# Kernel tuning notes

Measured on AMD Instinct MI355X. Metric: run time of the kernel, lower is better.

Reference implementation:

```python
import jax, jax.numpy as jnp
import numpy as np

B, H, W, D, SD, K, CD, ITERS = 16, 64, 64, 64, 64, 5, 8, 4
N = H * W
EPS = 1e-8
SCALE = SD ** -0.5

def _ln(x, g, b, eps=1e-5):
    m = jnp.mean(x, -1, keepdims=True)
    v = jnp.mean(jnp.square(x - m), -1, keepdims=True)
    return (x - m) * jax.lax.rsqrt(v + eps) * g + b

def _grid():
    xs = jnp.linspace(-1.0, 1.0, W)
    ys = jnp.linspace(-1.0, 1.0, H)
    yy, xx = jnp.meshgrid(ys, xs, indexing='ij')
    return jnp.stack([xx, yy], -1).reshape(N, 2)  # (N,2)

def _gru(x, h, wih, whh, bih, bhh):
    # PyTorch GRUCell: gates in (r, z, n) order
    gi = x @ wih.T + bih
    gh = h @ whh.T + bhh
    ir, iz, i_n = jnp.split(gi, 3, -1)
    hr, hz, h_n = jnp.split(gh, 3, -1)
    r = jax.nn.sigmoid(ir + hr)
    z = jax.nn.sigmoid(iz + hz)
    n = jnp.tanh(i_n + r * h_n)
    return (1.0 - z) * n + z * h

def _forward(p):
    grid = _grid()
    feat = _ln(p['feat'].reshape(B, N, D), p['ln_feat_g'], p['ln_feat_b'])
    fc = _ln(p['feat_color'], p['ln_fc_g'], p['ln_fc_b'])
    # background k/v: position-independent, computed once outside the loop
    ge_bg = jnp.concatenate([grid, -grid], -1) @ p['w_grid'].T + p['b_grid']  # (N,D)
    k_bg = _ln(feat @ p['w_kbg'].T + ge_bg, p['ln_bg_g'], p['ln_bg_b']) @ p['w_mlp_bg'].T + p['b_mlp_bg']
    v_bg = _ln(feat @ p['w_vbg'].T + ge_bg, p['ln_bg_g'], p['ln_bg_b']) @ p['w_mlp_bg'].T + p['b_mlp_bg']
    slot_fg = jnp.broadcast_to(p['slots_init_fg'], (B, K - 1, SD))
    slot_bg = jnp.broadcast_to(p['slots_init_bg'], (B, 1, SD))
    pos = jnp.broadcast_to(p['fg_position'], (B, K - 1, 2))
    kf = feat @ p['w_kfg'].T  # position-independent fg parts
    vf = feat @ p['w_vfg'].T
    for it in range(ITERS):
        q_fg = _ln(slot_fg, p['ln_q_g'], p['ln_q_b']) @ p['w_q'].T          # (B,K-1,SD)
        q_bg = _ln(slot_bg, p['ln_qbg_g'], p['ln_qbg_b']) @ p['w_qbg'].T    # (B,1,SD)
        rel = grid[None, None] - pos[:, :, None]                            # (B,K-1,N,2)
        ge = jnp.concatenate([rel, -rel], -1) @ p['w_grid'].T + p['b_grid'] # (B,K-1,N,D)
        k = _ln(kf[:, None] + ge, p['ln_fg_g'], p['ln_fg_b']) @ p['w_mlp_fg'].T + p['b_mlp_fg']
        v = _ln(vf[:, None] + ge, p['ln_fg_g'], p['ln_fg_b']) @ p['w_mlp_fg'].T + p['b_mlp_fg']
        a_fg = jnp.einsum('bkd,bknd->bkn', q_fg, k) * SCALE
        a_bg = jnp.einsum('bd,bnd->bn', q_bg[:, 0], k_bg) * SCALE
        # non-standard softmax: normalize across slot axis (K), not tokens
        attn = jax.nn.softmax(jnp.concatenate([a_bg[:, None], a_fg], 1), axis=1) + EPS
        w_fg = attn[:, 1:] / jnp.sum(attn[:, 1:], -1, keepdims=True)        # (B,K-1,N)
        w_bg = attn[:, :1] / jnp.sum(attn[:, :1], -1, keepdims=True)        # (B,1,N)
        pos = jnp.einsum('bkn,nd->bkd', w_fg, grid)
        pos = jnp.clip(pos + jnp.tanh(w_fg @ p['w_pos'].T + p['b_pos']) / 5.0, -1.0, 1.0)
        if it != ITERS - 1:
            upd_fg = jnp.einsum('bkn,bknd->bkd', w_fg, v)
            upd_bg = jnp.einsum('bkn,bnd->bkd', w_bg, v_bg)
            slot_fg = _gru(upd_fg.reshape(-1, SD), slot_fg.reshape(-1, SD),
                           p['gfg_wih'], p['gfg_whh'], p['gfg_bih'], p['gfg_bhh']).reshape(B, K - 1, SD)
            slot_fg = slot_fg + _ln(slot_fg, p['ln_rfg_g'], p['ln_rfg_b']) @ p['w_rfg'].T + p['b_rfg']
            slot_bg = _gru(upd_bg.reshape(-1, SD), slot_bg.reshape(-1, SD),
                           p['gbg_wih'], p['gbg_whh'], p['gbg_bih'], p['gbg_bhh']).reshape(B, 1, SD)
            slot_bg = slot_bg + _ln(slot_bg, p['ln_rbg_g'], p['ln_rbg_b']) @ p['w_rbg'].T + p['b_rbg']
        else:
            # last iteration: slots = [visual update, color update]
            slot_fg = jnp.concatenate([jnp.einsum('bkn,bknd->bkd', w_fg, v),
                                       jnp.einsum('bkn,bnd->bkd', w_fg, fc)], -1)
            slot_bg = jnp.concatenate([jnp.einsum('bkn,bnd->bkd', w_bg, v_bg),
                                       jnp.einsum('bkn,bnd->bkd', w_bg, fc)], -1)
    return jnp.concatenate([slot_bg, slot_fg], 1)  # (B,K,SD+CD)

def setup_inputs():
    key = jax.random.key(0)
    ks = iter(jax.random.split(key, 64))
    def rn(shape, s=0.02):
        return jax.random.normal(next(ks), shape, dtype=jnp.float32) * s
    inp = {
        'feat': jax.random.normal(next(ks), (B, H, W, D), dtype=jnp.float32),
        'feat_color': jax.random.normal(next(ks), (B, N, CD), dtype=jnp.float32),
        'w_grid': rn((D, 4)), 'b_grid': rn((D,)),
        'w_kfg': rn((D, D)), 'w_vfg': rn((D, D)),
        'w_kbg': rn((D, D)), 'w_vbg': rn((D, D)),
        'ln_fg_g': jnp.ones((D,)), 'ln_fg_b': jnp.zeros((D,)),
        'w_mlp_fg': rn((SD, D)), 'b_mlp_fg': rn((SD,)),
        'ln_bg_g': jnp.ones((D,)), 'ln_bg_b': jnp.zeros((D,)),
        'w_mlp_bg': rn((SD, D)), 'b_mlp_bg': rn((SD,)),
        'slots_init_fg': rn((1, K - 1, SD), 0.5),
        'slots_init_bg': rn((1, 1, SD), 0.5),
        'fg_position': jax.random.uniform(next(ks), (1, K - 1, 2), dtype=jnp.float32, minval=-0.75, maxval=0.75),
        'w_pos': rn((2, N), 0.001), 'b_pos': jnp.zeros((2,)),
        'ln_q_g': jnp.ones((SD,)), 'ln_q_b': jnp.zeros((SD,)), 'w_q': rn((SD, SD)),
        'ln_qbg_g': jnp.ones((SD,)), 'ln_qbg_b': jnp.zeros((SD,)), 'w_qbg': rn((SD, SD)),
        'gfg_wih': rn((3 * SD, SD)), 'gfg_whh': rn((3 * SD, SD)),
        'gfg_bih': rn((3 * SD,)), 'gfg_bhh': rn((3 * SD,)),
        'gbg_wih': rn((3 * SD, SD)), 'gbg_whh': rn((3 * SD, SD)),
        'gbg_bih': rn((3 * SD,)), 'gbg_bhh': rn((3 * SD,)),
        'ln_rfg_g': jnp.ones((SD,)), 'ln_rfg_b': jnp.zeros((SD,)),
        'w_rfg': rn((SD, SD)), 'b_rfg': rn((SD,)),
        'ln_rbg_g': jnp.ones((SD,)), 'ln_rbg_b': jnp.zeros((SD,)),
        'w_rbg': rn((SD, SD)), 'b_rbg': rn((SD,)),
        'ln_feat_g': jnp.ones((D,)), 'ln_feat_b': jnp.zeros((D,)),
        'ln_fc_g': jnp.ones((CD,)), 'ln_fc_b': jnp.zeros((CD,)),
    }
    return inp

def reference(feat, feat_color, w_grid, b_grid, w_kfg, w_vfg, w_kbg, w_vbg,
              ln_fg_g, ln_fg_b, w_mlp_fg, b_mlp_fg, ln_bg_g, ln_bg_b, w_mlp_bg, b_mlp_bg,
              slots_init_fg, slots_init_bg, fg_position, w_pos, b_pos,
              ln_q_g, ln_q_b, w_q, ln_qbg_g, ln_qbg_b, w_qbg,
              gfg_wih, gfg_whh, gfg_bih, gfg_bhh, gbg_wih, gbg_whh, gbg_bih, gbg_bhh,
              ln_rfg_g, ln_rfg_b, w_rfg, b_rfg, ln_rbg_g, ln_rbg_b, w_rbg, b_rbg,
              ln_feat_g, ln_feat_b, ln_fc_g, ln_fc_b):
    p = dict(locals())
    return _forward(p)
```

## Files before the change

kernel.cpp:

```cpp
#include <hip/hip_runtime.h>
#include <math.h>
#include <stddef.h>

#define NB 16
#define ND 64
#define NN 4096
#define NCD 8
#define NITER 4
#define ATT_EPS 1e-8f
#define LNEPS 1e-5f
#define QSCALE 0.125f

static constexpr size_t SZ_MAT   = (size_t)NB*NN*ND;
static constexpr size_t OFF_UK   = 0;
static constexpr size_t OFF_CV0  = OFF_UK   + SZ_MAT;
static constexpr size_t OFF_XKBG = OFF_CV0  + SZ_MAT;
static constexpr size_t OFF_XVBG = OFF_XKBG + SZ_MAT;
static constexpr size_t OFF_SCAL = OFF_XVBG + SZ_MAT;
static constexpr size_t OFF_ACC  = OFF_SCAL + (size_t)NB*NN*8;
static constexpr size_t OFF_SFG  = OFF_ACC  + (size_t)NB*448;
static constexpr size_t OFF_SBG  = OFF_SFG  + (size_t)NB*256;
static constexpr size_t OFF_POS  = OFF_SBG  + (size_t)NB*64;
static constexpr size_t OFF_QW   = OFF_POS  + (size_t)NB*8;
static constexpr size_t OFF_QWBG = OFF_QW   + (size_t)NB*256;
static constexpr size_t OFF_QBBG = OFF_QWBG + (size_t)NB*64;
static constexpr size_t OFF_ABC  = OFF_QBBG + (size_t)NB;
static constexpr size_t OFF_CXG  = OFF_ABC  + (size_t)NB*16;
static constexpr size_t OFF_CYG  = OFF_CXG  + 64;
static constexpr size_t OFF_GS   = OFF_CYG  + 64;

#define A_S 0
#define A_W0 8
#define A_WX 12
#define A_WY 16
#define A_P 24
#define A_T 32
#define A_C 40
#define A_Y 80
#define A_YBG 336
#define ACC_STRIDE 448

__device__ __forceinline__ float g16sum(float x){
  x += __shfl_xor(x, 1);
  x += __shfl_xor(x, 2);
  x += __shfl_xor(x, 4);
  x += __shfl_xor(x, 8);
  return x;
}
__device__ __forceinline__ float wavesum(float x){
  x += __shfl_xor(x, 1);  x += __shfl_xor(x, 2);
  x += __shfl_xor(x, 4);  x += __shfl_xor(x, 8);
  x += __shfl_xor(x, 16); x += __shfl_xor(x, 32);
  return x;
}
__device__ __forceinline__ float4 f4fma(float a, float4 w, float4 c){
  c.x = fmaf(a, w.x, c.x); c.y = fmaf(a, w.y, c.y);
  c.z = fmaf(a, w.z, c.z); c.w = fmaf(a, w.w, c.w);
  return c;
}
__device__ __forceinline__ float dot4(float4 a, float4 b){
  return fmaf(a.x,b.x, fmaf(a.y,b.y, fmaf(a.z,b.z, a.w*b.w)));
}
__device__ __forceinline__ float4 ln16v(float4 x, float4 g, float4 bb){
  float m = g16sum(x.x + x.y + x.z + x.w) * (1.0f/64.0f);
  float4 c = make_float4(x.x - m, x.y - m, x.z - m, x.w - m);
  float var = g16sum(c.x*c.x + c.y*c.y + c.z*c.z + c.w*c.w) * (1.0f/64.0f);
  float rs = rsqrtf(var + LNEPS);
  return make_float4(c.x*rs*g.x + bb.x, c.y*rs*g.y + bb.y,
                     c.z*rs*g.z + bb.z, c.w*rs*g.w + bb.w);
}
__device__ __forceinline__ float rowdot64(const float* __restrict__ W, const float* x){
  const float4* w4 = (const float4*)W;
  const float4* x4 = (const float4*)x;
  float s = 0.0f;
  #pragma unroll
  for (int t = 0; t < 16; ++t){
    float4 w = w4[t], xx = x4[t];
    s = fmaf(w.x,xx.x, fmaf(w.y,xx.y, fmaf(w.z,xx.z, fmaf(w.w,xx.w, s))));
  }
  return s;
}
#define XRED(x) do { x += __shfl_xor(x, 16); x += __shfl_xor(x, 32); } while (0)

__global__ __launch_bounds__(256) void k_pre(
    const float* __restrict__ feat,
    const float* __restrict__ w_kfg, const float* __restrict__ w_vfg,
    const float* __restrict__ w_kbg, const float* __restrict__ w_vbg,
    const float* __restrict__ w_grid, const float* __restrict__ b_grid,
    const float* __restrict__ ln_feat_g, const float* __restrict__ ln_feat_b,
    const float* __restrict__ ln_bg_g, const float* __restrict__ ln_bg_b,
    const float* __restrict__ ln_fg_g,
    float* __restrict__ ws)
{
  __shared__ float fl[64][68];
  __shared__ float wl[2][64][68];
  const int tid  = threadIdx.x;
  const int bid  = blockIdx.x;
  const int half = bid >> 10;
  const int tb   = bid & 1023;
  const int i    = tid >> 4;
  const int j    = tid & 15;
  const int e0j  = 4*j;
  const float* wA = half ? w_kbg : w_kfg;
  const float* wB = half ? w_vbg : w_vfg;

  #pragma unroll
  for (int it = 0; it < 8; ++it){
    const int f = it*256 + tid;
    const int m = f >> 10;
    const int r = f & 1023;
    const int d = r >> 4;
    const int s4 = r & 15;
    const float* src = m ? wB : wA;
    const float4 wv = *(const float4*)(src + d*64 + 4*s4);
    wl[m][4*s4+0][d] = wv.x;
    wl[m][4*s4+1][d] = wv.y;
    wl[m][4*s4+2][d] = wv.z;
    wl[m][4*s4+3][d] = wv.w;
  }
  {
    const float4 lfg4 = *(const float4*)(ln_feat_g + e0j);
    const float4 lfb4 = *(const float4*)(ln_feat_b + e0j);
    #pragma unroll
    for (int it = 0; it < 4; ++it){
      const int tok = it*16 + i;
      const size_t gb = ((size_t)tb*64 + tok)*64 + e0j;
      const float4 f4 = *(const float4*)(feat + gb);
      *(float4*)&fl[tok][e0j] = ln16v(f4, lfg4, lfb4);
    }
  }
  __syncthreads();

  float4 acc0[4], acc1[4];
  #pragma unroll
  for (int u = 0; u < 4; ++u){ acc0[u] = make_float4(0,0,0,0); acc1[u] = acc0[u]; }
  for (int e0 = 0; e0 < 64; e0 += 4){
    float4 a[4];
    #pragma unroll
    for (int u = 0; u < 4; ++u) a[u] = *(const float4*)&fl[u*16 + i][e0];
    #pragma unroll
    for (int l = 0; l < 4; ++l){
      const float4 b0 = *(const float4*)&wl[0][e0+l][e0j];
      const float4 b1 = *(const float4*)&wl[1][e0+l][e0j];
      #pragma unroll
      for (int u = 0; u < 4; ++u){
        const float av = l==0 ? a[u].x : l==1 ? a[u].y : l==2 ? a[u].z : a[u].w;
        acc0[u] = f4fma(av, b0, acc0[u]);
        acc1[u] = f4fma(av, b1, acc1[u]);
      }
    }
  }

  const float4 bgr4 = *(const float4*)(b_grid + e0j);
  float4 wgx4, wgy4;
  {
    float4 w0 = *(const float4*)(w_grid + (e0j+0)*4);
    float4 w1 = *(const float4*)(w_grid + (e0j+1)*4);
    float4 w2 = *(const float4*)(w_grid + (e0j+2)*4);
    float4 w3 = *(const float4*)(w_grid + (e0j+3)*4);
    wgx4 = make_float4(w0.x-w0.z, w1.x-w1.z, w2.x-w2.z, w3.x-w3.z);
    wgy4 = make_float4(w0.y-w0.w, w1.y-w1.w, w2.y-w2.w, w3.y-w3.w);
  }

  if (!half){
    const float4 lng4 = *(const float4*)(ln_fg_g + e0j);
    const float mx = g16sum(wgx4.x+wgx4.y+wgx4.z+wgx4.w)*(1.0f/64.0f);
    const float my = g16sum(wgy4.x+wgy4.y+wgy4.z+wgy4.w)*(1.0f/64.0f);
    const float4 cx4 = make_float4(wgx4.x-mx, wgx4.y-mx, wgx4.z-mx, wgx4.w-mx);
    const float4 cy4 = make_float4(wgy4.x-my, wgy4.y-my, wgy4.z-my, wgy4.w-my);
    float* uk  = ws + OFF_UK;
    float* cv0 = ws + OFF_CV0;
    #pragma unroll
    for (int u = 0; u < 4; ++u){
      const size_t t = (size_t)tb*64 + u*16 + i;
      const size_t fb = t*64 + e0j;
      float4 kb = make_float4(acc0[u].x+bgr4.x, acc0[u].y+bgr4.y, acc0[u].z+bgr4.z, acc0[u].w+bgr4.w);
      float mk = g16sum(kb.x+kb.y+kb.z+kb.w)*(1.0f/64.0f);
      float4 c0 = make_float4(kb.x-mk, kb.y-mk, kb.z-mk, kb.w-mk);
      float sk0 = g16sum(dot4(c0,c0));
      float skx = g16sum(dot4(c0,cx4));
      float sky = g16sum(dot4(c0,cy4));
      *(float4*)(uk + fb) = make_float4(c0.x*lng4.x, c0.y*lng4.y, c0.z*lng4.z, c0.w*lng4.w);
      float4 vb = make_float4(acc1[u].x+bgr4.x, acc1[u].y+bgr4.y, acc1[u].z+bgr4.z, acc1[u].w+bgr4.w);
      float mv = g16sum(vb.x+vb.y+vb.z+vb.w)*(1.0f/64.0f);
      float4 cv = make_float4(vb.x-mv, vb.y-mv, vb.z-mv, vb.w-mv);
      float sv0 = g16sum(dot4(cv,cv));
      float svx = g16sum(dot4(cv,cx4));
      float svy = g16sum(dot4(cv,cy4));
      *(float4*)(cv0 + fb) = cv;
      if (j == 0){
        float* sc = ws + OFF_SCAL + t*8;
        *(float4*)(sc)   = make_float4(sk0, 2.0f*skx, 2.0f*sky, 0.0f);
        *(float4*)(sc+4) = make_float4(sv0, 2.0f*svx, 2.0f*svy, 0.0f);
      }
    }
  } else {
    const float4 lbg4 = *(const float4*)(ln_bg_g + e0j);
    const float4 lbb4 = *(const float4*)(ln_bg_b + e0j);
    float* xkbg = ws + OFF_XKBG;
    float* xvbg = ws + OFF_XVBG;
    #pragma unroll
    for (int u = 0; u < 4; ++u){
      const size_t t = (size_t)tb*64 + u*16 + i;
      const int n = (int)(t & (NN-1));
      const float gx = -1.0f + (2.0f/63.0f)*(float)(n & 63);
      const float gy = -1.0f + (2.0f/63.0f)*(float)(n >> 6);
      const float4 ge = make_float4(
          fmaf(gx, wgx4.x, fmaf(gy, wgy4.x, bgr4.x)),
          fmaf(gx, wgx4.y, fmaf(gy, wgy4.y, bgr4.y)),
          fmaf(gx, wgx4.z, fmaf(gy, wgy4.z, bgr4.z)),
          fmaf(gx, wgx4.w, fmaf(gy, wgy4.w, bgr4.w)));
      const size_t fb = t*64 + e0j;
      float4 xk = make_float4(acc0[u].x+ge.x, acc0[u].y+ge.y, acc0[u].z+ge.z, acc0[u].w+ge.w);
      *(float4*)(xkbg + fb) = ln16v(xk, lbg4, lbb4);
      float4 xv = make_float4(acc1[u].x+ge.x, acc1[u].y+ge.y, acc1[u].z+ge.z, acc1[u].w+ge.w);
      *(float4*)(xvbg + fb) = ln16v(xv, lbg4, lbb4);
    }
  }
}

__global__ void k_init(const float* __restrict__ sfg0, const float* __restrict__ sbg0,
                       const float* __restrict__ pos0, const float* __restrict__ w_grid,
                       const float* __restrict__ ln_fg_g, float* __restrict__ ws){
  const int t = blockIdx.x*256 + threadIdx.x;
  if (t < NB*256) ws[OFF_SFG + t] = sfg0[t & 255];
  if (t < NB*64)  ws[OFF_SBG + t] = sbg0[t & 63];
  if (t < NB*8)   ws[OFF_POS + t] = pos0[t & 7];
  if (blockIdx.x == 0 && threadIdx.x < 64){
    const int d = threadIdx.x;
    const float wgx = w_grid[4*d] - w_grid[4*d+2];
    const float wgy = w_grid[4*d+1] - w_grid[4*d+3];
    const float mx = wavesum(wgx)*(1.0f/64.0f);
    const float my = wavesum(wgy)*(1.0f/64.0f);
    const float cx = wgx - mx, cy = wgy - my;
    ws[OFF_CXG + d] = cx*ln_fg_g[d];
    ws[OFF_CYG + d] = cy*ln_fg_g[d];
    const float gxx = wavesum(cx*cx);
    const float gyy = wavesum(cy*cy);
    const float gxy = wavesum(cx*cy);
    if (d == 0){ ws[OFF_GS] = gxx; ws[OFF_GS+1] = gyy; ws[OFF_GS+2] = 2.0f*gxy; }
  }
}

__global__ __launch_bounds__(64) void k_prep(
    const float* __restrict__ ln_q_g, const float* __restrict__ ln_q_b,
    const float* __restrict__ w_q,
    const float* __restrict__ ln_qbg_g, const float* __restrict__ ln_qbg_b,
    const float* __restrict__ w_qbg,
    const float* __restrict__ w_mlp_fg, const float* __restrict__ b_mlp_fg,
    const float* __restrict__ w_mlp_bg, const float* __restrict__ b_mlp_bg,
    const float* __restrict__ ln_fg_b,
    float* __restrict__ ws)
{
  const int k = blockIdx.x, b = blockIdx.y, d = threadIdx.x;
  __shared__ float qin[64], qv[64];
  if (k == 0){
    float* acc = ws + OFF_ACC + (size_t)b*ACC_STRIDE;
    for (int i2 = d; i2 < ACC_STRIDE; i2 += 64) acc[i2] = 0.0f;
  }
  if (k < 4){
    const float sv = ws[OFF_SFG + b*256 + k*64 + d];
    const float m = wavesum(sv)*(1.0f/64.0f);
    const float c = sv - m;
    const float var = wavesum(c*c)*(1.0f/64.0f);
    const float rs = rsqrtf(var + LNEPS);
    qin[d] = c*rs*ln_q_g[d] + ln_q_b[d];
    __syncthreads();
    const float q = rowdot64(w_q + d*64, qin);
    qv[d] = q;
    const float qb = wavesum(q * b_mlp_fg[d]);
    __syncthreads();
    float qw = 0.0f;
    for (int e = 0; e < 64; ++e) qw = fmaf(qv[e], w_mlp_fg[e*64+d], qw);
    ws[OFF_QW + b*256 + k*64 + d] = qw;
    const float A  = wavesum(qw * ws[OFF_CXG + d]);
    const float Bv = wavesum(qw * ws[OFF_CYG + d]);
    const float Cv = wavesum(qw * ln_fg_b[d]) + qb;
    if (d == 0){
      float* abc = ws + OFF_ABC + (size_t)(b*4 + k)*4;
      abc[0] = A; abc[1] = Bv; abc[2] = Cv;
    }
  } else {
    const float sv = ws[OFF_SBG + b*64 + d];
    const float m = wavesum(sv)*(1.0f/64.0f);
    const float c = sv - m;
    const float var = wavesum(c*c)*(1.0f/64.0f);
    const float rs = rsqrtf(var + LNEPS);
    qin[d] = c*rs*ln_qbg_g[d] + ln_qbg_b[d];
    __syncthreads();
    const float q = rowdot64(w_qbg + d*64, qin);
    qv[d] = q;
    const float qb = wavesum(q * b_mlp_bg[d]);
    __syncthreads();
    float qw = 0.0f;
    for (int e = 0; e < 64; ++e) qw = fmaf(qv[e], w_mlp_bg[e*64+d], qw);
    ws[OFF_QWBG + b*64 + d] = qw;
    if (d == 0) ws[OFF_QBBG + b] = qb;
  }
}

template<int LAST>
__global__ __launch_bounds__(256) void k_main(
    const float* __restrict__ fc, const float* __restrict__ fcg,
    const float* __restrict__ fcb, const float* __restrict__ w_pos,
    float* __restrict__ ws)
{
  __shared__ float red[ACC_STRIDE];
  const int tid = threadIdx.x;
  const int b = blockIdx.y;
  for (int i2 = tid; i2 < ACC_STRIDE; i2 += 256) red[i2] = 0.0f;
  __syncthreads();

  const int G = tid >> 4;
  const int s = tid & 15;
  const int e0 = 4*s;

  float4 qw4[4]; float A[4], Bc[4], Cc[4], px[4], py[4];
  #pragma unroll
  for (int k = 0; k < 4; ++k){
    qw4[k] = *(const float4*)(ws + OFF_QW + (size_t)b*256 + k*64 + e0);
    const float* abc = ws + OFF_ABC + (size_t)(b*4 + k)*4;
    A[k] = abc[0]; Bc[k] = abc[1]; Cc[k] = abc[2];
    px[k] = ws[OFF_POS + b*8 + k*2 + 0];
    py[k] = ws[OFF_POS + b*8 + k*2 + 1];
  }
  const float4 qwbg4 = *(const float4*)(ws + OFF_QWBG + (size_t)b*64 + e0);
  const float qbbg = ws[OFF_QBBG + b];
  const float Gxx = ws[OFF_GS], Gyy = ws[OFF_GS+1], Gxy2 = ws[OFF_GS+2];

  const float* uk   = ws + OFF_UK;
  const float* cv0  = ws + OFF_CV0;
  const float* xkbg = ws + OFF_XKBG;
  const float* xvbg = ws + OFF_XVBG;

  float accY[4][4] = {};
  float accYbg[4] = {};
  float accS[5] = {};
  float accW0[4] = {}, accWx[4] = {}, accWy[4] = {};
  float accP[4][2] = {};
  float accT[4][2] = {};
  float accC[5] = {};

  const int nbase = blockIdx.x*64 + G*4;
  for (int i = 0; i < 4; ++i){
    const int n = nbase + i;
    const size_t tok = ((size_t)b << 12) + (size_t)n;
    const size_t rbase = tok*64 + e0;
    const float4 uk4  = *(const float4*)(uk + rbase);
    const float4 cv4  = *(const float4*)(cv0 + rbase);
    const float4 xkb4 = *(const float4*)(xkbg + rbase);
    const float4 xvb4 = *(const float4*)(xvbg + rbase);
    const float4 sA = *(const float4*)(ws + OFF_SCAL + tok*8);
    const float4 sB = *(const float4*)(ws + OFF_SCAL + tok*8 + 4);
    const float gx = -1.0f + (2.0f/63.0f)*(float)(n & 63);
    const float gy = -1.0f + (2.0f/63.0f)*(float)(n >> 6);
    float fcv = 0.0f, wpx = 0.0f, wpy = 0.0f;
    if (LAST){
      float v = (s < 8) ? fc[tok*8 + s] : 0.0f;
      float m8 = v;
      m8 += __shfl_xor(m8, 1); m8 += __shfl_xor(m8, 2); m8 += __shfl_xor(m8, 4);
      m8 *= 0.125f;
      const float cc = v - m8;
      float va = cc*cc;
      va += __shfl_xor(va, 1); va += __shfl_xor(va, 2); va += __shfl_xor(va, 4);
      va *= 0.125f;
      const float rs8 = rsqrtf(va + LNEPS);
      fcv = (s < 8) ? cc*rs8*fcg[s] + fcb[s] : 0.0f;
    } else {
      wpx = w_pos[n]; wpy = w_pos[NN + n];
    }

    float a0 = g16sum(dot4(xkb4, qwbg4));
    a0 = QSCALE*(a0 + qbbg);

    float a[4], rsv[4];
    #pragma unroll
    for (int k = 0; k < 4; ++k){
      const float rx = gx - px[k];
      const float ry = gy - py[k];
      const float rxy = rx*ry;
      float h1 = fmaf(rx, Gxx, sA.y);
      float h2 = fmaf(ry, Gyy, sA.z);
      float vk = fmaf(rx, h1, fmaf(ry, h2, sA.x));
      vk = fmaf(rxy, Gxy2, vk);
      const float rsk = rsqrtf(fmaf(vk, 1.0f/64.0f, LNEPS));
      float h1v = fmaf(rx, Gxx, sB.y);
      float h2v = fmaf(ry, Gyy, sB.z);
      float vv = fmaf(rx, h1v, fmaf(ry, h2v, sB.x));
      vv = fmaf(rxy, Gxy2, vv);
      rsv[k] = rsqrtf(fmaf(vv, 1.0f/64.0f, LNEPS));
      float dk = g16sum(dot4(uk4, qw4[k]));
      dk = fmaf(rx, A[k], dk);
      dk = fmaf(ry, Bc[k], dk);
      a[k] = QSCALE * fmaf(rsk, dk, Cc[k]);
    }
    const float mx = fmaxf(fmaxf(fmaxf(a[0],a[1]), fmaxf(a[2],a[3])), a0);
    float p0 = __expf(a0 - mx);
    float pk[4];
    float sum = p0;
    #pragma unroll
    for (int k = 0; k < 4; ++k){ pk[k] = __expf(a[k]-mx); sum += pk[k]; }
    const float inv = 1.0f/sum;
    p0 = fmaf(p0, inv, ATT_EPS);
    #pragma unroll
    for (int k = 0; k < 4; ++k) pk[k] = fmaf(pk[k], inv, ATT_EPS);

    accS[0] += p0;
    accYbg[0] = fmaf(p0, xvb4.x, accYbg[0]);
    accYbg[1] = fmaf(p0, xvb4.y, accYbg[1]);
    accYbg[2] = fmaf(p0, xvb4.z, accYbg[2]);
    accYbg[3] = fmaf(p0, xvb4.w, accYbg[3]);
    if (LAST) accC[0] = fmaf(p0, fcv, accC[0]);
    #pragma unroll
    for (int k = 0; k < 4; ++k){
      accS[k+1] += pk[k];
      const float prv = pk[k]*rsv[k];
      accY[k][0] = fmaf(prv, cv4.x, accY[k][0]);
      accY[k][1] = fmaf(prv, cv4.y, accY[k][1]);
      accY[k][2] = fmaf(prv, cv4.z, accY[k][2]);
      accY[k][3] = fmaf(prv, cv4.w, accY[k][3]);
      accW0[k] += prv;
      accWx[k] = fmaf(prv, gx, accWx[k]);
      accWy[k] = fmaf(prv, gy, accWy[k]);
      if (LAST){
        accC[k+1] = fmaf(pk[k], fcv, accC[k+1]);
      } else {
        accP[k][0] = fmaf(pk[k], gx, accP[k][0]);
        accP[k][1] = fmaf(pk[k], gy, accP[k][1]);
        accT[k][0] = fmaf(pk[k], wpx, accT[k][0]);
        accT[k][1] = fmaf(pk[k], wpy, accT[k][1]);
      }
    }
  }

  #pragma unroll
  for (int k = 0; k < 4; ++k){
    #pragma unroll
    for (int j2 = 0; j2 < 4; ++j2){ float x = accY[k][j2]; XRED(x); accY[k][j2] = x; }
    float x;
    x = accW0[k]; XRED(x); accW0[k] = x;
    x = accWx[k]; XRED(x); accWx[k] = x;
    x = accWy[k]; XRED(x); accWy[k] = x;
    x = accP[k][0]; XRED(x); accP[k][0] = x;
    x = accP[k][1]; XRED(x); accP[k][1] = x;
    x = accT[k][0]; XRED(x); accT[k][0] = x;
    x = accT[k][1]; XRED(x); accT[k][1] = x;
  }
  #pragma unroll
  for (int j2 = 0; j2 < 4; ++j2){ float x = accYbg[j2]; XRED(x); accYbg[j2] = x; }
  #pragma unroll
  for (int sl = 0; sl < 5; ++sl){ float x = accS[sl]; XRED(x); accS[sl] = x; }
  #pragma unroll
  for (int sl = 0; sl < 5; ++sl){ float x = accC[sl]; XRED(x); accC[sl] = x; }

  const bool g0 = (G & 3) == 0;
  if (g0){
    #pragma unroll
    for (int k = 0; k < 4; ++k){
      atomicAdd(&red[A_Y + k*64 + e0 + 0], accY[k][0]);
      atomicAdd(&red[A_Y + k*64 + e0 + 1], accY[k][1]);
      atomicAdd(&red[A_Y + k*64 + e0 + 2], accY[k][2]);
      atomicAdd(&red[A_Y + k*64 + e0 + 3], accY[k][3]);
    }
    atomicAdd(&red[A_YBG + e0 + 0], accYbg[0]);
    atomicAdd(&red[A_YBG + e0 + 1], accYbg[1]);
    atomicAdd(&red[A_YBG + e0 + 2], accYbg[2]);
    atomicAdd(&red[A_YBG + e0 + 3], accYbg[3]);
    if (s == 0){
      #pragma unroll
      for (int sl = 0; sl < 5; ++sl) atomicAdd(&red[A_S + sl], accS[sl]);
      #pragma unroll
      for (int k = 0; k < 4; ++k){
        atomicAdd(&red[A_W0 + k], accW0[k]);
        atomicAdd(&red[A_WX + k], accWx[k]);
        atomicAdd(&red[A_WY + k], accWy[k]);
      }
      if (!LAST){
        #pragma unroll
        for (int k = 0; k < 4; ++k){
          atomicAdd(&red[A_P + k*2 + 0], accP[k][0]);
          atomicAdd(&red[A_P + k*2 + 1], accP[k][1]);
          atomicAdd(&red[A_T + k*2 + 0], accT[k][0]);
          atomicAdd(&red[A_T + k*2 + 1], accT[k][1]);
        }
      }
    }
    if (LAST && s < 8){
      #pragma unroll
      for (int sl = 0; sl < 5; ++sl) atomicAdd(&red[A_C + sl*8 + s], accC[sl]);
    }
  }
  __syncthreads();
  float* gacc = ws + OFF_ACC + (size_t)b*ACC_STRIDE;
  for (int i2 = tid; i2 < ACC_STRIDE; i2 += 256){
    const float v = red[i2];
    if (v != 0.0f) atomicAdd(&gacc[i2], v);
  }
}

__global__ __launch_bounds__(64) void k_update(
    const float* __restrict__ w_mlp_fg, const float* __restrict__ b_mlp_fg,
    const float* __restrict__ w_mlp_bg, const float* __restrict__ b_mlp_bg,
    const float* __restrict__ gfg_wih, const float* __restrict__ gfg_whh,
    const float* __restrict__ gfg_bih, const float* __restrict__ gfg_bhh,
    const float* __restrict__ gbg_wih, const float* __restrict__ gbg_whh,
    const float* __restrict__ gbg_bih, const float* __restrict__ gbg_bhh,
    const float* __restrict__ ln_rfg_g, const float* __restrict__ ln_rfg_b,
    const float* __restrict__ w_rfg, const float* __restrict__ b_rfg,
    const float* __restrict__ ln_rbg_g, const float* __restrict__ ln_rbg_b,
    const float* __restrict__ w_rbg, const float* __restrict__ b_rbg,
    const float* __restrict__ b_pos,
    const float* __restrict__ ln_fg_g, const float* __restrict__ ln_fg_b,
    float* __restrict__ ws)
{
  const int k = blockIdx.x, b = blockIdx.y, d = threadIdx.x;
  float* acc = ws + OFF_ACC + (size_t)b*ACC_STRIDE;
  __shared__ float xl[64], hl[64], rl[64];
  if (k < 4){
    const float invS = 1.0f/acc[A_S + 1 + k];
    const float pxv = ws[OFF_POS + b*8 + k*2 + 0];
    const float pyv = ws[OFF_POS + b*8 + k*2 + 1];
    const float wxc = (acc[A_WX + k] - pxv*acc[A_W0 + k])*invS;
    const float wyc = (acc[A_WY + k] - pyv*acc[A_W0 + k])*invS;
    xl[d] = acc[A_Y + k*64 + d]*invS*ln_fg_g[d]
          + wxc*ws[OFF_CXG + d] + wyc*ws[OFF_CYG + d] + ln_fg_b[d];
    const float h = ws[OFF_SFG + b*256 + k*64 + d];
    hl[d] = h;
    __syncthreads();
    const float upd = b_mlp_fg[d] + rowdot64(w_mlp_fg + d*64, xl);
    __syncthreads();
    xl[d] = upd;
    __syncthreads();
    const float gir = gfg_bih[d]     + rowdot64(gfg_wih + d*64, xl);
    const float giz = gfg_bih[64+d]  + rowdot64(gfg_wih + (64+d)*64, xl);
    const float gin = gfg_bih[128+d] + rowdot64(gfg_wih + (128+d)*64, xl);
    const float ghr = gfg_bhh[d]     + rowdot64(gfg_whh + d*64, hl);
    const float ghz = gfg_bhh[64+d]  + rowdot64(gfg_whh + (64+d)*64, hl);
    const float ghn = gfg_bhh[128+d] + rowdot64(gfg_whh + (128+d)*64, hl);
    const float r = 1.0f/(1.0f + expf(-(gir+ghr)));
    const float z = 1.0f/(1.0f + expf(-(giz+ghz)));
    const float nng = tanhf(fmaf(r, ghn, gin));
    const float hnew = (1.0f - z)*nng + z*h;
    const float m = wavesum(hnew)*(1.0f/64.0f);
    const float c = hnew - m;
    const float var = wavesum(c*c)*(1.0f/64.0f);
    const float rs = rsqrtf(var + LNEPS);
    rl[d] = c*rs*ln_rfg_g[d] + ln_rfg_b[d];
    __syncthreads();
    const float outv = hnew + b_rfg[d] + rowdot64(w_rfg + d*64, rl);
    ws[OFF_SFG + b*256 + k*64 + d] = outv;
    if (d < 2){
      const float P = acc[A_P + k*2 + d]*invS;
      const float T = acc[A_T + k*2 + d]*invS;
      float pn = P + tanhf(T + b_pos[d])*0.2f;
      pn = fminf(1.0f, fmaxf(-1.0f, pn));
      ws[OFF_POS + b*8 + k*2 + d] = pn;
    }
  } else {
    const float invS = 1.0f/acc[A_S];
    xl[d] = acc[A_YBG + d]*invS;
    const float h = ws[OFF_SBG + b*64 + d];
    hl[d] = h;
    __syncthreads();
    const float upd = b_mlp_bg[d] + rowdot64(w_mlp_bg + d*64, xl);
    __syncthreads();
    xl[d] = upd;
    __syncthreads();
    const float gir = gbg_bih[d]     + rowdot64(gbg_wih + d*64, xl);
    const float giz = gbg_bih[64+d]  + rowdot64(gbg_wih + (64+d)*64, xl);
    const float gin = gbg_bih[128+d] + rowdot64(gbg_wih + (128+d)*64, xl);
    const float ghr = gbg_bhh[d]     + rowdot64(gbg_whh + d*64, hl);
    const float ghz = gbg_bhh[64+d]  + rowdot64(gbg_whh + (64+d)*64, hl);
    const float ghn = gbg_bhh[128+d] + rowdot64(gbg_whh + (128+d)*64, hl);
    const float r = 1.0f/(1.0f + expf(-(gir+ghr)));
    const float z = 1.0f/(1.0f + expf(-(giz+ghz)));
    const float nng = tanhf(fmaf(r, ghn, gin));
    const float hnew = (1.0f - z)*nng + z*h;
    const float m = wavesum(hnew)*(1.0f/64.0f);
    const float c = hnew - m;
    const float var = wavesum(c*c)*(1.0f/64.0f);
    const float rs = rsqrtf(var + LNEPS);
    rl[d] = c*rs*ln_rbg_g[d] + ln_rbg_b[d];
    __syncthreads();
    const float outv = hnew + b_rbg[d] + rowdot64(w_rbg + d*64, rl);
    ws[OFF_SBG + b*64 + d] = outv;
  }
}

__global__ __launch_bounds__(64) void k_final(
    const float* __restrict__ w_mlp_fg, const float* __restrict__ b_mlp_fg,
    const float* __restrict__ w_mlp_bg, const float* __restrict__ b_mlp_bg,
    const float* __restrict__ ln_fg_g, const float* __restrict__ ln_fg_b,
    const float* __restrict__ ws, float* __restrict__ out)
{
  const int k = blockIdx.x, b = blockIdx.y, d = threadIdx.x;
  const float* acc = ws + OFF_ACC + (size_t)b*ACC_STRIDE;
  __shared__ float xl[64];
  if (k < 4){
    const float invS = 1.0f/acc[A_S + 1 + k];
    const float pxv = ws[OFF_POS + b*8 + k*2 + 0];
    const float pyv = ws[OFF_POS + b*8 + k*2 + 1];
    const float wxc = (acc[A_WX + k] - pxv*acc[A_W0 + k])*invS;
    const float wyc = (acc[A_WY + k] - pyv*acc[A_W0 + k])*invS;
    xl[d] = acc[A_Y + k*64 + d]*invS*ln_fg_g[d]
          + wxc*ws[OFF_CXG + d] + wyc*ws[OFF_CYG + d] + ln_fg_b[d];
    __syncthreads();
    const float o = b_mlp_fg[d] + rowdot64(w_mlp_fg + d*64, xl);
    out[(size_t)(b*5 + 1 + k)*72 + d] = o;
    if (d < 8) out[(size_t)(b*5 + 1 + k)*72 + 64 + d] = acc[A_C + (k+1)*8 + d]*invS;
  } else {
    const float invS = 1.0f/acc[A_S];
    xl[d] = acc[A_YBG + d]*invS;
    __syncthreads();
    const float o = b_mlp_bg[d] + rowdot64(w_mlp_bg + d*64, xl);
    out[(size_t)(b*5)*72 + d] = o;
    if (d < 8) out[(size_t)(b*5)*72 + 64 + d] = acc[A_C + d]*invS;
  }
}

extern "C" void kernel_launch(void* const* d_in, const int* in_sizes, int n_in,
                              void* d_out, int out_size, void* d_ws, size_t ws_size,
                              hipStream_t stream)
{
  const float* feat          = (const float*)d_in[0];
  const float* feat_color    = (const float*)d_in[1];
  const float* w_grid        = (const float*)d_in[2];
  const float* b_grid        = (const float*)d_in[3];
  const float* w_kfg         = (const float*)d_in[4];
  const float* w_vfg         = (const float*)d_in[5];
  const float* w_kbg         = (const float*)d_in[6];
  const float* w_vbg         = (const float*)d_in[7];
  const float* ln_fg_g       = (const float*)d_in[8];
  const float* ln_fg_b       = (const float*)d_in[9];
  const float* w_mlp_fg      = (const float*)d_in[10];
  const float* b_mlp_fg      = (const float*)d_in[11];
  const float* ln_bg_g       = (const float*)d_in[12];
  const float* ln_bg_b       = (const float*)d_in[13];
  const float* w_mlp_bg      = (const float*)d_in[14];
  const float* b_mlp_bg      = (const float*)d_in[15];
  const float* slots_init_fg = (const float*)d_in[16];
  const float* slots_init_bg = (const float*)d_in[17];
  const float* fg_position   = (const float*)d_in[18];
  const float* w_pos         = (const float*)d_in[19];
  const float* b_pos         = (const float*)d_in[20];
  const float* ln_q_g        = (const float*)d_in[21];
  const float* ln_q_b        = (const float*)d_in[22];
  const float* w_q           = (const float*)d_in[23];
  const float* ln_qbg_g      = (const float*)d_in[24];
  const float* ln_qbg_b      = (const float*)d_in[25];
  const float* w_qbg         = (const float*)d_in[26];
  const float* gfg_wih       = (const float*)d_in[27];
  const float* gfg_whh       = (const float*)d_in[28];
  const float* gfg_bih       = (const float*)d_in[29];
  const float* gfg_bhh       = (const float*)d_in[30];
  const float* gbg_wih       = (const float*)d_in[31];
  const float* gbg_whh       = (const float*)d_in[32];
  const float* gbg_bih       = (const float*)d_in[33];
  const float* gbg_bhh       = (const float*)d_in[34];
  const float* ln_rfg_g      = (const float*)d_in[35];
  const float* ln_rfg_b      = (const float*)d_in[36];
  const float* w_rfg         = (const float*)d_in[37];
  const float* b_rfg         = (const float*)d_in[38];
  const float* ln_rbg_g      = (const float*)d_in[39];
  const float* ln_rbg_b      = (const float*)d_in[40];
  const float* w_rbg         = (const float*)d_in[41];
  const float* b_rbg         = (const float*)d_in[42];
  const float* ln_feat_g     = (const float*)d_in[43];
  const float* ln_feat_b     = (const float*)d_in[44];
  const float* ln_fc_g       = (const float*)d_in[45];
  const float* ln_fc_b       = (const float*)d_in[46];
  float* ws  = (float*)d_ws;
  float* out = (float*)d_out;

  hipLaunchKernelGGL(k_pre, dim3(2048), dim3(256), 0, stream,
                     feat, w_kfg, w_vfg, w_kbg, w_vbg, w_grid, b_grid,
                     ln_feat_g, ln_feat_b, ln_bg_g, ln_bg_b, ln_fg_g, ws);
  hipLaunchKernelGGL(k_init, dim3(16), dim3(256), 0, stream,
                     slots_init_fg, slots_init_bg, fg_position, w_grid, ln_fg_g, ws);
  for (int it = 0; it < NITER; ++it){
    hipLaunchKernelGGL(k_prep, dim3(5,16), dim3(64), 0, stream,
                       ln_q_g, ln_q_b, w_q, ln_qbg_g, ln_qbg_b, w_qbg,
                       w_mlp_fg, b_mlp_fg, w_mlp_bg, b_mlp_bg, ln_fg_b, ws);
    if (it < NITER-1){
      hipLaunchKernelGGL((k_main<0>), dim3(64,16), dim3(256), 0, stream,
                         feat_color, ln_fc_g, ln_fc_b, w_pos, ws);
      hipLaunchKernelGGL(k_update, dim3(5,16), dim3(64), 0, stream,
                         w_mlp_fg, b_mlp_fg, w_mlp_bg, b_mlp_bg,
                         gfg_wih, gfg_whh, gfg_bih, gfg_bhh,
                         gbg_wih, gbg_whh, gbg_bih, gbg_bhh,
                         ln_rfg_g, ln_rfg_b, w_rfg, b_rfg,
                         ln_rbg_g, ln_rbg_b, w_rbg, b_rbg,
                         b_pos, ln_fg_g, ln_fg_b, ws);
    } else {
      hipLaunchKernelGGL((k_main<1>), dim3(64,16), dim3(256), 0, stream,
                         feat_color, ln_fc_g, ln_fc_b, w_pos, ws);
      hipLaunchKernelGGL(k_final, dim3(5,16), dim3(64), 0, stream,
                         w_mlp_fg, b_mlp_fg, w_mlp_bg, b_mlp_bg,
                         ln_fg_g, ln_fg_b, ws, out);
    }
  }
}
```

Before: 204.0 us.

## Fuse query prep into slot update, double-buffer accumulators, trim k_pre LDS

```diff
diff --git a/kernel.cpp b/kernel.cpp
--- a/kernel.cpp
+++ b/kernel.cpp
@@ -18,16 +18,14 @@
 static constexpr size_t OFF_XVBG = OFF_XKBG + SZ_MAT;
 static constexpr size_t OFF_SCAL = OFF_XVBG + SZ_MAT;
 static constexpr size_t OFF_ACC  = OFF_SCAL + (size_t)NB*NN*8;
-static constexpr size_t OFF_SFG  = OFF_ACC  + (size_t)NB*448;
+static constexpr size_t OFF_SFG  = OFF_ACC  + (size_t)NB*2*448;
 static constexpr size_t OFF_SBG  = OFF_SFG  + (size_t)NB*256;
 static constexpr size_t OFF_POS  = OFF_SBG  + (size_t)NB*64;
 static constexpr size_t OFF_QW   = OFF_POS  + (size_t)NB*8;
 static constexpr size_t OFF_QWBG = OFF_QW   + (size_t)NB*256;
 static constexpr size_t OFF_QBBG = OFF_QWBG + (size_t)NB*64;
 static constexpr size_t OFF_ABC  = OFF_QBBG + (size_t)NB;
-static constexpr size_t OFF_CXG  = OFF_ABC  + (size_t)NB*16;
-static constexpr size_t OFF_CYG  = OFF_CXG  + 64;
-static constexpr size_t OFF_GS   = OFF_CYG  + 64;
+static constexpr size_t OFF_GS   = OFF_ABC  + (size_t)NB*16;
 
 #define A_S 0
 #define A_W0 8
@@ -69,20 +67,34 @@
   return make_float4(c.x*rs*g.x + bb.x, c.y*rs*g.y + bb.y,
                      c.z*rs*g.z + bb.z, c.w*rs*g.w + bb.w);
 }
-__device__ __forceinline__ float rowdot64(const float* __restrict__ W, const float* x){
+__device__ __forceinline__ float rowdot64f(const float* __restrict__ W, const float* x){
   const float4* w4 = (const float4*)W;
   const float4* x4 = (const float4*)x;
-  float s = 0.0f;
+  float s0=0.f, s1=0.f, s2=0.f, s3=0.f;
+  #pragma unroll
+  for (int t = 0; t < 4; ++t){
+    float4 w, xx;
+    w = w4[t];     xx = x4[t];     s0 = fmaf(w.x,xx.x, fmaf(w.y,xx.y, fmaf(w.z,xx.z, fmaf(w.w,xx.w, s0))));
+    w = w4[4+t];   xx = x4[4+t];   s1 = fmaf(w.x,xx.x, fmaf(w.y,xx.y, fmaf(w.z,xx.z, fmaf(w.w,xx.w, s1))));
+    w = w4[8+t];   xx = x4[8+t];   s2 = fmaf(w.x,xx.x, fmaf(w.y,xx.y, fmaf(w.z,xx.z, fmaf(w.w,xx.w, s2))));
+    w = w4[12+t];  xx = x4[12+t];  s3 = fmaf(w.x,xx.x, fmaf(w.y,xx.y, fmaf(w.z,xx.z, fmaf(w.w,xx.w, s3))));
+  }
+  return (s0+s1)+(s2+s3);
+}
+__device__ __forceinline__ float coldot64(const float* __restrict__ W, const float* x, int d){
+  float s0=0.f, s1=0.f, s2=0.f, s3=0.f;
   #pragma unroll
   for (int t = 0; t < 16; ++t){
-    float4 w = w4[t], xx = x4[t];
-    s = fmaf(w.x,xx.x, fmaf(w.y,xx.y, fmaf(w.z,xx.z, fmaf(w.w,xx.w, s))));
-  }
-  return s;
+    s0 = fmaf(x[t],      W[(t)*64+d],      s0);
+    s1 = fmaf(x[16+t],   W[(16+t)*64+d],   s1);
+    s2 = fmaf(x[32+t],   W[(32+t)*64+d],   s2);
+    s3 = fmaf(x[48+t],   W[(48+t)*64+d],   s3);
+  }
+  return (s0+s1)+(s2+s3);
 }
 #define XRED(x) do { x += __shfl_xor(x, 16); x += __shfl_xor(x, 32); } while (0)
 
-__global__ __launch_bounds__(256) void k_pre(
+__global__ __launch_bounds__(256, 4) void k_pre(
     const float* __restrict__ feat,
     const float* __restrict__ w_kfg, const float* __restrict__ w_vfg,
     const float* __restrict__ w_kbg, const float* __restrict__ w_vbg,
@@ -92,8 +104,8 @@
     const float* __restrict__ ln_fg_g,
     float* __restrict__ ws)
 {
-  __shared__ float fl[64][68];
-  __shared__ float wl[2][64][68];
+  __shared__ __align__(16) float fl[64][68];
+  __shared__ __align__(16) float wl[64][68];
   const int tid  = threadIdx.x;
   const int bid  = blockIdx.x;
   const int half = bid >> 10;
@@ -101,23 +113,7 @@
   const int i    = tid >> 4;
   const int j    = tid & 15;
   const int e0j  = 4*j;
-  const float* wA = half ? w_kbg : w_kfg;
-  const float* wB = half ? w_vbg : w_vfg;
-
-  #pragma unroll
-  for (int it = 0; it < 8; ++it){
-    const int f = it*256 + tid;
-    const int m = f >> 10;
-    const int r = f & 1023;
-    const int d = r >> 4;
-    const int s4 = r & 15;
-    const float* src = m ? wB : wA;
-    const float4 wv = *(const float4*)(src + d*64 + 4*s4);
-    wl[m][4*s4+0][d] = wv.x;
-    wl[m][4*s4+1][d] = wv.y;
-    wl[m][4*s4+2][d] = wv.z;
-    wl[m][4*s4+3][d] = wv.w;
-  }
+
   {
     const float4 lfg4 = *(const float4*)(ln_feat_g + e0j);
     const float4 lfb4 = *(const float4*)(ln_feat_b + e0j);
@@ -127,27 +123,6 @@
       const size_t gb = ((size_t)tb*64 + tok)*64 + e0j;
       const float4 f4 = *(const float4*)(feat + gb);
       *(float4*)&fl[tok][e0j] = ln16v(f4, lfg4, lfb4);
-    }
-  }
-  __syncthreads();
-
-  float4 acc0[4], acc1[4];
-  #pragma unroll
-  for (int u = 0; u < 4; ++u){ acc0[u] = make_float4(0,0,0,0); acc1[u] = acc0[u]; }
-  for (int e0 = 0; e0 < 64; e0 += 4){
-    float4 a[4];
-    #pragma unroll
-    for (int u = 0; u < 4; ++u) a[u] = *(const float4*)&fl[u*16 + i][e0];
-    #pragma unroll
-    for (int l = 0; l < 4; ++l){
-      const float4 b0 = *(const float4*)&wl[0][e0+l][e0j];
-      const float4 b1 = *(const float4*)&wl[1][e0+l][e0j];
-      #pragma unroll
-      for (int u = 0; u < 4; ++u){
-        const float av = l==0 ? a[u].x : l==1 ? a[u].y : l==2 ? a[u].z : a[u].w;
-        acc0[u] = f4fma(av, b0, acc0[u]);
-        acc1[u] = f4fma(av, b1, acc1[u]);
-      }
     }
   }
 
@@ -161,139 +136,166 @@
     wgx4 = make_float4(w0.x-w0.z, w1.x-w1.z, w2.x-w2.z, w3.x-w3.z);
     wgy4 = make_float4(w0.y-w0.w, w1.y-w1.w, w2.y-w2.w, w3.y-w3.w);
   }
-
+  float4 cx4 = make_float4(0,0,0,0), cy4 = cx4, lng4 = cx4;
+  float4 lbg4 = cx4, lbb4 = cx4, ge[4];
   if (!half){
-    const float4 lng4 = *(const float4*)(ln_fg_g + e0j);
+    lng4 = *(const float4*)(ln_fg_g + e0j);
     const float mx = g16sum(wgx4.x+wgx4.y+wgx4.z+wgx4.w)*(1.0f/64.0f);
     const float my = g16sum(wgy4.x+wgy4.y+wgy4.z+wgy4.w)*(1.0f/64.0f);
-    const float4 cx4 = make_float4(wgx4.x-mx, wgx4.y-mx, wgx4.z-mx, wgx4.w-mx);
-    const float4 cy4 = make_float4(wgy4.x-my, wgy4.y-my, wgy4.z-my, wgy4.w-my);
-    float* uk  = ws + OFF_UK;
-    float* cv0 = ws + OFF_CV0;
-    #pragma unroll
-    for (int u = 0; u < 4; ++u){
-      const size_t t = (size_t)tb*64 + u*16 + i;
-      const size_t fb = t*64 + e0j;
-      float4 kb = make_float4(acc0[u].x+bgr4.x, acc0[u].y+bgr4.y, acc0[u].z+bgr4.z, acc0[u].w+bgr4.w);
-      float mk = g16sum(kb.x+kb.y+kb.z+kb.w)*(1.0f/64.0f);
-      float4 c0 = make_float4(kb.x-mk, kb.y-mk, kb.z-mk, kb.w-mk);
-      float sk0 = g16sum(dot4(c0,c0));
-      float skx = g16sum(dot4(c0,cx4));
-      float sky = g16sum(dot4(c0,cy4));
-      *(float4*)(uk + fb) = make_float4(c0.x*lng4.x, c0.y*lng4.y, c0.z*lng4.z, c0.w*lng4.w);
-      float4 vb = make_float4(acc1[u].x+bgr4.x, acc1[u].y+bgr4.y, acc1[u].z+bgr4.z, acc1[u].w+bgr4.w);
-      float mv = g16sum(vb.x+vb.y+vb.z+vb.w)*(1.0f/64.0f);
-      float4 cv = make_float4(vb.x-mv, vb.y-mv, vb.z-mv, vb.w-mv);
-      float sv0 = g16sum(dot4(cv,cv));
-      float svx = g16sum(dot4(cv,cx4));
-      float svy = g16sum(dot4(cv,cy4));
-      *(float4*)(cv0 + fb) = cv;
-      if (j == 0){
-        float* sc = ws + OFF_SCAL + t*8;
-        *(float4*)(sc)   = make_float4(sk0, 2.0f*skx, 2.0f*sky, 0.0f);
-        *(float4*)(sc+4) = make_float4(sv0, 2.0f*svx, 2.0f*svy, 0.0f);
-      }
-    }
+    cx4 = make_float4(wgx4.x-mx, wgx4.y-mx, wgx4.z-mx, wgx4.w-mx);
+    cy4 = make_float4(wgy4.x-my, wgy4.y-my, wgy4.z-my, wgy4.w-my);
   } else {
-    const float4 lbg4 = *(const float4*)(ln_bg_g + e0j);
-    const float4 lbb4 = *(const float4*)(ln_bg_b + e0j);
-    float* xkbg = ws + OFF_XKBG;
-    float* xvbg = ws + OFF_XVBG;
+    lbg4 = *(const float4*)(ln_bg_g + e0j);
+    lbb4 = *(const float4*)(ln_bg_b + e0j);
     #pragma unroll
     for (int u = 0; u < 4; ++u){
       const size_t t = (size_t)tb*64 + u*16 + i;
       const int n = (int)(t & (NN-1));
       const float gx = -1.0f + (2.0f/63.0f)*(float)(n & 63);
       const float gy = -1.0f + (2.0f/63.0f)*(float)(n >> 6);
-      const float4 ge = make_float4(
+      ge[u] = make_float4(
           fmaf(gx, wgx4.x, fmaf(gy, wgy4.x, bgr4.x)),
           fmaf(gx, wgx4.y, fmaf(gy, wgy4.y, bgr4.y)),
           fmaf(gx, wgx4.z, fmaf(gy, wgy4.z, bgr4.z)),
           fmaf(gx, wgx4.w, fmaf(gy, wgy4.w, bgr4.w)));
-      const size_t fb = t*64 + e0j;
-      float4 xk = make_float4(acc0[u].x+ge.x, acc0[u].y+ge.y, acc0[u].z+ge.z, acc0[u].w+ge.w);
-      *(float4*)(xkbg + fb) = ln16v(xk, lbg4, lbb4);
-      float4 xv = make_float4(acc1[u].x+ge.x, acc1[u].y+ge.y, acc1[u].z+ge.z, acc1[u].w+ge.w);
-      *(float4*)(xvbg + fb) = ln16v(xv, lbg4, lbb4);
-    }
-  }
-}
-
-__global__ void k_init(const float* __restrict__ sfg0, const float* __restrict__ sbg0,
-                       const float* __restrict__ pos0, const float* __restrict__ w_grid,
-                       const float* __restrict__ ln_fg_g, float* __restrict__ ws){
-  const int t = blockIdx.x*256 + threadIdx.x;
-  if (t < NB*256) ws[OFF_SFG + t] = sfg0[t & 255];
-  if (t < NB*64)  ws[OFF_SBG + t] = sbg0[t & 63];
-  if (t < NB*8)   ws[OFF_POS + t] = pos0[t & 7];
-  if (blockIdx.x == 0 && threadIdx.x < 64){
-    const int d = threadIdx.x;
-    const float wgx = w_grid[4*d] - w_grid[4*d+2];
-    const float wgy = w_grid[4*d+1] - w_grid[4*d+3];
-    const float mx = wavesum(wgx)*(1.0f/64.0f);
-    const float my = wavesum(wgy)*(1.0f/64.0f);
-    const float cx = wgx - mx, cy = wgy - my;
-    ws[OFF_CXG + d] = cx*ln_fg_g[d];
-    ws[OFF_CYG + d] = cy*ln_fg_g[d];
-    const float gxx = wavesum(cx*cx);
-    const float gyy = wavesum(cy*cy);
-    const float gxy = wavesum(cx*cy);
-    if (d == 0){ ws[OFF_GS] = gxx; ws[OFF_GS+1] = gyy; ws[OFF_GS+2] = 2.0f*gxy; }
-  }
-}
-
-__global__ __launch_bounds__(64) void k_prep(
+    }
+  }
+
+  for (int m = 0; m < 2; ++m){
+    const float* src = half ? (m ? w_vbg : w_kbg) : (m ? w_vfg : w_kfg);
+    #pragma unroll
+    for (int it = 0; it < 4; ++it){
+      const int f = it*256 + tid;
+      const int d = f >> 4;
+      const int s4 = f & 15;
+      const float4 wv = *(const float4*)(src + d*64 + 4*s4);
+      wl[4*s4+0][d] = wv.x;
+      wl[4*s4+1][d] = wv.y;
+      wl[4*s4+2][d] = wv.z;
+      wl[4*s4+3][d] = wv.w;
+    }
+    __syncthreads();
+
+    float4 acc[4];
+    #pragma unroll
+    for (int u = 0; u < 4; ++u) acc[u] = make_float4(0,0,0,0);
+    for (int e0 = 0; e0 < 64; e0 += 4){
+      float4 a[4];
+      #pragma unroll
+      for (int u = 0; u < 4; ++u) a[u] = *(const float4*)&fl[u*16 + i][e0];
+      #pragma unroll
+      for (int l = 0; l < 4; ++l){
+        const float4 bb = *(const float4*)&wl[e0+l][e0j];
+        #pragma unroll
+        for (int u = 0; u < 4; ++u){
+          const float av = l==0 ? a[u].x : l==1 ? a[u].y : l==2 ? a[u].z : a[u].w;
+          acc[u] = f4fma(av, bb, acc[u]);
+        }
+      }
+    }
+
+    if (!half){
+      float* dst = ws + (m ? OFF_CV0 : OFF_UK);
+      #pragma unroll
+      for (int u = 0; u < 4; ++u){
+        const size_t t = (size_t)tb*64 + u*16 + i;
+        const size_t fb = t*64 + e0j;
+        float4 kb = make_float4(acc[u].x+bgr4.x, acc[u].y+bgr4.y, acc[u].z+bgr4.z, acc[u].w+bgr4.w);
+        float mk = g16sum(kb.x+kb.y+kb.z+kb.w)*(1.0f/64.0f);
+        float4 c0 = make_float4(kb.x-mk, kb.y-mk, kb.z-mk, kb.w-mk);
+        float s00 = g16sum(dot4(c0,c0));
+        float s0x = g16sum(dot4(c0,cx4));
+        float s0y = g16sum(dot4(c0,cy4));
+        if (m == 0){
+          *(float4*)(dst + fb) = make_float4(c0.x*lng4.x, c0.y*lng4.y, c0.z*lng4.z, c0.w*lng4.w);
+        } else {
+          *(float4*)(dst + fb) = c0;
+        }
+        if (j == 0){
+          *(float4*)(ws + OFF_SCAL + t*8 + 4*m) = make_float4(s00, 2.0f*s0x, 2.0f*s0y, 0.0f);
+        }
+      }
+    } else {
+      float* dst = ws + (m ? OFF_XVBG : OFF_XKBG);
+      #pragma unroll
+      for (int u = 0; u < 4; ++u){
+        const size_t t = (size_t)tb*64 + u*16 + i;
+        const size_t fb = t*64 + e0j;
+        float4 xk = make_float4(acc[u].x+ge[u].x, acc[u].y+ge[u].y, acc[u].z+ge[u].z, acc[u].w+ge[u].w);
+        *(float4*)(dst + fb) = ln16v(xk, lbg4, lbb4);
+      }
+    }
+    __syncthreads();
+  }
+}
+
+__global__ __launch_bounds__(64) void k_init0(
+    const float* __restrict__ sfg0, const float* __restrict__ sbg0,
+    const float* __restrict__ pos0, const float* __restrict__ w_grid,
+    const float* __restrict__ ln_fg_g, const float* __restrict__ ln_fg_b,
     const float* __restrict__ ln_q_g, const float* __restrict__ ln_q_b,
     const float* __restrict__ w_q,
     const float* __restrict__ ln_qbg_g, const float* __restrict__ ln_qbg_b,
     const float* __restrict__ w_qbg,
     const float* __restrict__ w_mlp_fg, const float* __restrict__ b_mlp_fg,
     const float* __restrict__ w_mlp_bg, const float* __restrict__ b_mlp_bg,
-    const float* __restrict__ ln_fg_b,
     float* __restrict__ ws)
 {
   const int k = blockIdx.x, b = blockIdx.y, d = threadIdx.x;
-  __shared__ float qin[64], qv[64];
-  if (k == 0){
-    float* acc = ws + OFF_ACC + (size_t)b*ACC_STRIDE;
-    for (int i2 = d; i2 < ACC_STRIDE; i2 += 64) acc[i2] = 0.0f;
-  }
+  __shared__ __align__(16) float xl[64], hl[64];
+  const float wgx = w_grid[4*d] - w_grid[4*d+2];
+  const float wgy = w_grid[4*d+1] - w_grid[4*d+3];
+  const float mgx = wavesum(wgx)*(1.0f/64.0f);
+  const float mgy = wavesum(wgy)*(1.0f/64.0f);
+  const float cx = wgx - mgx, cy = wgy - mgy;
+
   if (k < 4){
-    const float sv = ws[OFF_SFG + b*256 + k*64 + d];
+    const float sv = sfg0[k*64 + d];
+    ws[OFF_SFG + b*256 + k*64 + d] = sv;
+    if (d < 2) ws[OFF_POS + b*8 + k*2 + d] = pos0[k*2 + d];
+    const float cxg = cx*ln_fg_g[d];
+    const float cyg = cy*ln_fg_g[d];
     const float m = wavesum(sv)*(1.0f/64.0f);
     const float c = sv - m;
     const float var = wavesum(c*c)*(1.0f/64.0f);
     const float rs = rsqrtf(var + LNEPS);
-    qin[d] = c*rs*ln_q_g[d] + ln_q_b[d];
-    __syncthreads();
-    const float q = rowdot64(w_q + d*64, qin);
-    qv[d] = q;
+    xl[d] = c*rs*ln_q_g[d] + ln_q_b[d];
+    __syncthreads();
+    const float q = rowdot64f(w_q + d*64, xl);
+    hl[d] = q;
     const float qb = wavesum(q * b_mlp_fg[d]);
     __syncthreads();
-    float qw = 0.0f;
-    for (int e = 0; e < 64; ++e) qw = fmaf(qv[e], w_mlp_fg[e*64+d], qw);
+    const float qw = coldot64(w_mlp_fg, hl, d);
     ws[OFF_QW + b*256 + k*64 + d] = qw;
-    const float A  = wavesum(qw * ws[OFF_CXG + d]);
-    const float Bv = wavesum(qw * ws[OFF_CYG + d]);
+    const float A  = wavesum(qw * cxg);
+    const float Bv = wavesum(qw * cyg);
     const float Cv = wavesum(qw * ln_fg_b[d]) + qb;
     if (d == 0){
       float* abc = ws + OFF_ABC + (size_t)(b*4 + k)*4;
       abc[0] = A; abc[1] = Bv; abc[2] = Cv;
     }
   } else {
-    const float sv = ws[OFF_SBG + b*64 + d];
+    const float sv = sbg0[d];
+    ws[OFF_SBG + b*64 + d] = sv;
+    float* accb = ws + OFF_ACC + (size_t)b*2*ACC_STRIDE;
+    for (int i2 = d; i2 < 2*ACC_STRIDE; i2 += 64) accb[i2] = 0.0f;
+    if (b == 0){
+      const float gxx = wavesum(cx*cx);
+      const float gyy = wavesum(cy*cy);
+      const float gxy = wavesum(cx*cy);
+      if (d == 0){ ws[OFF_GS] = gxx; ws[OFF_GS+1] = gyy; ws[OFF_GS+2] = 2.0f*gxy; }
+    }
     const float m = wavesum(sv)*(1.0f/64.0f);
     const float c = sv - m;
     const float var = wavesum(c*c)*(1.0f/64.0f);
     const float rs = rsqrtf(var + LNEPS);
-    qin[d] = c*rs*ln_qbg_g[d] + ln_qbg_b[d];
-    __syncthreads();
-    const float q = rowdot64(w_qbg + d*64, qin);
-    qv[d] = q;
+    xl[d] = c*rs*ln_qbg_g[d] + ln_qbg_b[d];
+    __syncthreads();
+    const float q = rowdot64f(w_qbg + d*64, xl);
+    hl[d] = q;
     const float qb = wavesum(q * b_mlp_bg[d]);
     __syncthreads();
-    float qw = 0.0f;
-    for (int e = 0; e < 64; ++e) qw = fmaf(qv[e], w_mlp_bg[e*64+d], qw);
+    const float qw = coldot64(w_mlp_bg, hl, d);
     ws[OFF_QWBG + b*64 + d] = qw;
     if (d == 0) ws[OFF_QBBG + b] = qb;
   }
@@ -303,7 +305,7 @@
 __global__ __launch_bounds__(256) void k_main(
     const float* __restrict__ fc, const float* __restrict__ fcg,
     const float* __restrict__ fcb, const float* __restrict__ w_pos,
-    float* __restrict__ ws)
+    float* __restrict__ ws, int bank)
 {
   __shared__ float red[ACC_STRIDE];
   const int tid = threadIdx.x;
@@ -491,14 +493,14 @@
     }
   }
   __syncthreads();
-  float* gacc = ws + OFF_ACC + (size_t)b*ACC_STRIDE;
+  float* gacc = ws + OFF_ACC + ((size_t)b*2 + bank)*ACC_STRIDE;
   for (int i2 = tid; i2 < ACC_STRIDE; i2 += 256){
     const float v = red[i2];
     if (v != 0.0f) atomicAdd(&gacc[i2], v);
   }
 }
 
-__global__ __launch_bounds__(64) void k_update(
+__global__ __launch_bounds__(64) void k_slotupd(
     const float* __restrict__ w_mlp_fg, const float* __restrict__ b_mlp_fg,
     const float* __restrict__ w_mlp_bg, const float* __restrict__ b_mlp_bg,
     const float* __restrict__ gfg_wih, const float* __restrict__ gfg_whh,
@@ -511,32 +513,44 @@
     const float* __restrict__ w_rbg, const float* __restrict__ b_rbg,
     const float* __restrict__ b_pos,
     const float* __restrict__ ln_fg_g, const float* __restrict__ ln_fg_b,
-    float* __restrict__ ws)
+    const float* __restrict__ ln_q_g, const float* __restrict__ ln_q_b,
+    const float* __restrict__ w_q,
+    const float* __restrict__ ln_qbg_g, const float* __restrict__ ln_qbg_b,
+    const float* __restrict__ w_qbg,
+    const float* __restrict__ w_grid,
+    float* __restrict__ ws, int rbank)
 {
   const int k = blockIdx.x, b = blockIdx.y, d = threadIdx.x;
-  float* acc = ws + OFF_ACC + (size_t)b*ACC_STRIDE;
-  __shared__ float xl[64], hl[64], rl[64];
+  float* accR = ws + OFF_ACC + ((size_t)b*2 + rbank)*ACC_STRIDE;
+  float* accZ = ws + OFF_ACC + ((size_t)b*2 + (rbank^1))*ACC_STRIDE;
+  __shared__ __align__(16) float xl[64], hl[64], rl[64];
+
   if (k < 4){
-    const float invS = 1.0f/acc[A_S + 1 + k];
+    const float wgx = w_grid[4*d] - w_grid[4*d+2];
+    const float wgy = w_grid[4*d+1] - w_grid[4*d+3];
+    const float mgx = wavesum(wgx)*(1.0f/64.0f);
+    const float mgy = wavesum(wgy)*(1.0f/64.0f);
+    const float cxg = (wgx - mgx)*ln_fg_g[d];
+    const float cyg = (wgy - mgy)*ln_fg_g[d];
+    const float invS = 1.0f/accR[A_S + 1 + k];
     const float pxv = ws[OFF_POS + b*8 + k*2 + 0];
     const float pyv = ws[OFF_POS + b*8 + k*2 + 1];
-    const float wxc = (acc[A_WX + k] - pxv*acc[A_W0 + k])*invS;
-    const float wyc = (acc[A_WY + k] - pyv*acc[A_W0 + k])*invS;
-    xl[d] = acc[A_Y + k*64 + d]*invS*ln_fg_g[d]
-          + wxc*ws[OFF_CXG + d] + wyc*ws[OFF_CYG + d] + ln_fg_b[d];
+    const float wxc = (accR[A_WX + k] - pxv*accR[A_W0 + k])*invS;
+    const float wyc = (accR[A_WY + k] - pyv*accR[A_W0 + k])*invS;
+    xl[d] = accR[A_Y + k*64 + d]*invS*ln_fg_g[d] + wxc*cxg + wyc*cyg + ln_fg_b[d];
     const float h = ws[OFF_SFG + b*256 + k*64 + d];
     hl[d] = h;
     __syncthreads();
-    const float upd = b_mlp_fg[d] + rowdot64(w_mlp_fg + d*64, xl);
+    const float upd = b_mlp_fg[d] + rowdot64f(w_mlp_fg + d*64, xl);
     __syncthreads();
     xl[d] = upd;
     __syncthreads();
-    const float gir = gfg_bih[d]     + rowdot64(gfg_wih + d*64, xl);
-    const float giz = gfg_bih[64+d]  + rowdot64(gfg_wih + (64+d)*64, xl);
-    const float gin = gfg_bih[128+d] + rowdot64(gfg_wih + (128+d)*64, xl);
-    const float ghr = gfg_bhh[d]     + rowdot64(gfg_whh + d*64, hl);
-    const float ghz = gfg_bhh[64+d]  + rowdot64(gfg_whh + (64+d)*64, hl);
-    const float ghn = gfg_bhh[128+d] + rowdot64(gfg_whh + (128+d)*64, hl);
+    const float gir = gfg_bih[d]     + rowdot64f(gfg_wih + d*64, xl);
+    const float giz = gfg_bih[64+d]  + rowdot64f(gfg_wih + (64+d)*64, xl);
+    const float gin = gfg_bih[128+d] + rowdot64f(gfg_wih + (128+d)*64, xl);
+    const float ghr = gfg_bhh[d]     + rowdot64f(gfg_whh + d*64, hl);
+    const float ghz = gfg_bhh[64+d]  + rowdot64f(gfg_whh + (64+d)*64, hl);
+    const float ghn = gfg_bhh[128+d] + rowdot64f(gfg_whh + (128+d)*64, hl);
     const float r = 1.0f/(1.0f + expf(-(gir+ghr)));
     const float z = 1.0f/(1.0f + expf(-(giz+ghz)));
     const float nng = tanhf(fmaf(r, ghn, gin));
@@ -547,31 +561,50 @@
     const float rs = rsqrtf(var + LNEPS);
     rl[d] = c*rs*ln_rfg_g[d] + ln_rfg_b[d];
     __syncthreads();
-    const float outv = hnew + b_rfg[d] + rowdot64(w_rfg + d*64, rl);
-    ws[OFF_SFG + b*256 + k*64 + d] = outv;
+    const float snew = hnew + b_rfg[d] + rowdot64f(w_rfg + d*64, rl);
+    ws[OFF_SFG + b*256 + k*64 + d] = snew;
     if (d < 2){
-      const float P = acc[A_P + k*2 + d]*invS;
-      const float T = acc[A_T + k*2 + d]*invS;
+      const float P = accR[A_P + k*2 + d]*invS;
+      const float T = accR[A_T + k*2 + d]*invS;
       float pn = P + tanhf(T + b_pos[d])*0.2f;
       pn = fminf(1.0f, fmaxf(-1.0f, pn));
       ws[OFF_POS + b*8 + k*2 + d] = pn;
     }
+    const float m2 = wavesum(snew)*(1.0f/64.0f);
+    const float c2 = snew - m2;
+    const float var2 = wavesum(c2*c2)*(1.0f/64.0f);
+    const float rs2 = rsqrtf(var2 + LNEPS);
+    xl[d] = c2*rs2*ln_q_g[d] + ln_q_b[d];
+    __syncthreads();
+    const float q = rowdot64f(w_q + d*64, xl);
+    hl[d] = q;
+    const float qb = wavesum(q * b_mlp_fg[d]);
+    __syncthreads();
+    const float qw = coldot64(w_mlp_fg, hl, d);
+    ws[OFF_QW + b*256 + k*64 + d] = qw;
+    const float A  = wavesum(qw * cxg);
+    const float Bv = wavesum(qw * cyg);
+    const float Cv = wavesum(qw * ln_fg_b[d]) + qb;
+    if (d == 0){
+      float* abc = ws + OFF_ABC + (size_t)(b*4 + k)*4;
+      abc[0] = A; abc[1] = Bv; abc[2] = Cv;
+    }
   } else {
-    const float invS = 1.0f/acc[A_S];
-    xl[d] = acc[A_YBG + d]*invS;
+    const float invS = 1.0f/accR[A_S];
+    xl[d] = accR[A_YBG + d]*invS;
     const float h = ws[OFF_SBG + b*64 + d];
     hl[d] = h;
     __syncthreads();
-    const float upd = b_mlp_bg[d] + rowdot64(w_mlp_bg + d*64, xl);
+    const float upd = b_mlp_bg[d] + rowdot64f(w_mlp_bg + d*64, xl);
     __syncthreads();
     xl[d] = upd;
     __syncthreads();
-    const float gir = gbg_bih[d]     + rowdot64(gbg_wih + d*64, xl);
-    const float giz = gbg_bih[64+d]  + rowdot64(gbg_wih + (64+d)*64, xl);
-    const float gin = gbg_bih[128+d] + rowdot64(gbg_wih + (128+d)*64, xl);
-    const float ghr = gbg_bhh[d]     + rowdot64(gbg_whh + d*64, hl);
-    const float ghz = gbg_bhh[64+d]  + rowdot64(gbg_whh + (64+d)*64, hl);
-    const float ghn = gbg_bhh[128+d] + rowdot64(gbg_whh + (128+d)*64, hl);
+    const float gir = gbg_bih[d]     + rowdot64f(gbg_wih + d*64, xl);
+    const float giz = gbg_bih[64+d]  + rowdot64f(gbg_wih + (64+d)*64, xl);
+    const float gin = gbg_bih[128+d] + rowdot64f(gbg_wih + (128+d)*64, xl);
+    const float ghr = gbg_bhh[d]     + rowdot64f(gbg_whh + d*64, hl);
+    const float ghz = gbg_bhh[64+d]  + rowdot64f(gbg_whh + (64+d)*64, hl);
+    const float ghn = gbg_bhh[128+d] + rowdot64f(gbg_whh + (128+d)*64, hl);
     const float r = 1.0f/(1.0f + expf(-(gir+ghr)));
     const float z = 1.0f/(1.0f + expf(-(giz+ghz)));
     const float nng = tanhf(fmaf(r, ghn, gin));
@@ -582,8 +615,22 @@
     const float rs = rsqrtf(var + LNEPS);
     rl[d] = c*rs*ln_rbg_g[d] + ln_rbg_b[d];
     __syncthreads();
-    const float outv = hnew + b_rbg[d] + rowdot64(w_rbg + d*64, rl);
-    ws[OFF_SBG + b*64 + d] = outv;
+    const float snew = hnew + b_rbg[d] + rowdot64f(w_rbg + d*64, rl);
+    ws[OFF_SBG + b*64 + d] = snew;
+    const float m2 = wavesum(snew)*(1.0f/64.0f);
+    const float c2 = snew - m2;
+    const float var2 = wavesum(c2*c2)*(1.0f/64.0f);
+    const float rs2 = rsqrtf(var2 + LNEPS);
+    xl[d] = c2*rs2*ln_qbg_g[d] + ln_qbg_b[d];
+    __syncthreads();
+    const float q = rowdot64f(w_qbg + d*64, xl);
+    hl[d] = q;
+    const float qb = wavesum(q * b_mlp_bg[d]);
+    __syncthreads();
+    const float qw = coldot64(w_mlp_bg, hl, d);
+    ws[OFF_QWBG + b*64 + d] = qw;
+    if (d == 0) ws[OFF_QBBG + b] = qb;
+    for (int i2 = d; i2 < ACC_STRIDE; i2 += 64) accZ[i2] = 0.0f;
   }
 }
 
@@ -591,28 +638,34 @@
     const float* __restrict__ w_mlp_fg, const float* __restrict__ b_mlp_fg,
     const float* __restrict__ w_mlp_bg, const float* __restrict__ b_mlp_bg,
     const float* __restrict__ ln_fg_g, const float* __restrict__ ln_fg_b,
+    const float* __restrict__ w_grid,
     const float* __restrict__ ws, float* __restrict__ out)
 {
   const int k = blockIdx.x, b = blockIdx.y, d = threadIdx.x;
-  const float* acc = ws + OFF_ACC + (size_t)b*ACC_STRIDE;
-  __shared__ float xl[64];
+  const float* acc = ws + OFF_ACC + ((size_t)b*2 + 1)*ACC_STRIDE;
+  __shared__ __align__(16) float xl[64];
   if (k < 4){
+    const float wgx = w_grid[4*d] - w_grid[4*d+2];
+    const float wgy = w_grid[4*d+1] - w_grid[4*d+3];
+    const float mgx = wavesum(wgx)*(1.0f/64.0f);
+    const float mgy = wavesum(wgy)*(1.0f/64.0f);
+    const float cxg = (wgx - mgx)*ln_fg_g[d];
+    const float cyg = (wgy - mgy)*ln_fg_g[d];
     const float invS = 1.0f/acc[A_S + 1 + k];
     const float pxv = ws[OFF_POS + b*8 + k*2 + 0];
     const float pyv = ws[OFF_POS + b*8 + k*2 + 1];
     const float wxc = (acc[A_WX + k] - pxv*acc[A_W0 + k])*invS;
     const float wyc = (acc[A_WY + k] - pyv*acc[A_W0 + k])*invS;
-    xl[d] = acc[A_Y + k*64 + d]*invS*ln_fg_g[d]
-          + wxc*ws[OFF_CXG + d] + wyc*ws[OFF_CYG + d] + ln_fg_b[d];
-    __syncthreads();
-    const float o = b_mlp_fg[d] + rowdot64(w_mlp_fg + d*64, xl);
+    xl[d] = acc[A_Y + k*64 + d]*invS*ln_fg_g[d] + wxc*cxg + wyc*cyg + ln_fg_b[d];
+    __syncthreads();
+    const float o = b_mlp_fg[d] + rowdot64f(w_mlp_fg + d*64, xl);
     out[(size_t)(b*5 + 1 + k)*72 + d] = o;
     if (d < 8) out[(size_t)(b*5 + 1 + k)*72 + 64 + d] = acc[A_C + (k+1)*8 + d]*invS;
   } else {
     const float invS = 1.0f/acc[A_S];
     xl[d] = acc[A_YBG + d]*invS;
     __syncthreads();
-    const float o = b_mlp_bg[d] + rowdot64(w_mlp_bg + d*64, xl);
+    const float o = b_mlp_bg[d] + rowdot64f(w_mlp_bg + d*64, xl);
     out[(size_t)(b*5)*72 + d] = o;
     if (d < 8) out[(size_t)(b*5)*72 + 64 + d] = acc[A_C + d]*invS;
   }
@@ -672,31 +725,34 @@
   float* ws  = (float*)d_ws;
   float* out = (float*)d_out;
 
+  hipLaunchKernelGGL(k_init0, dim3(5,16), dim3(64), 0, stream,
+                     slots_init_fg, slots_init_bg, fg_position, w_grid,
+                     ln_fg_g, ln_fg_b, ln_q_g, ln_q_b, w_q,
+                     ln_qbg_g, ln_qbg_b, w_qbg,
+                     w_mlp_fg, b_mlp_fg, w_mlp_bg, b_mlp_bg, ws);
   hipLaunchKernelGGL(k_pre, dim3(2048), dim3(256), 0, stream,
                      feat, w_kfg, w_vfg, w_kbg, w_vbg, w_grid, b_grid,
                      ln_feat_g, ln_feat_b, ln_bg_g, ln_bg_b, ln_fg_g, ws);
-  hipLaunchKernelGGL(k_init, dim3(16), dim3(256), 0, stream,
-                     slots_init_fg, slots_init_bg, fg_position, w_grid, ln_fg_g, ws);
   for (int it = 0; it < NITER; ++it){
-    hipLaunchKernelGGL(k_prep, dim3(5,16), dim3(64), 0, stream,
-                       ln_q_g, ln_q_b, w_q, ln_qbg_g, ln_qbg_b, w_qbg,
-                       w_mlp_fg, b_mlp_fg, w_mlp_bg, b_mlp_bg, ln_fg_b, ws);
+    const int bank = it & 1;
     if (it < NITER-1){
       hipLaunchKernelGGL((k_main<0>), dim3(64,16), dim3(256), 0, stream,
-                         feat_color, ln_fc_g, ln_fc_b, w_pos, ws);
-      hipLaunchKernelGGL(k_update, dim3(5,16), dim3(64), 0, stream,
+                         feat_color, ln_fc_g, ln_fc_b, w_pos, ws, bank);
+      hipLaunchKernelGGL(k_slotupd, dim3(5,16), dim3(64), 0, stream,
                          w_mlp_fg, b_mlp_fg, w_mlp_bg, b_mlp_bg,
                          gfg_wih, gfg_whh, gfg_bih, gfg_bhh,
                          gbg_wih, gbg_whh, gbg_bih, gbg_bhh,
                          ln_rfg_g, ln_rfg_b, w_rfg, b_rfg,
                          ln_rbg_g, ln_rbg_b, w_rbg, b_rbg,
-                         b_pos, ln_fg_g, ln_fg_b, ws);
+                         b_pos, ln_fg_g, ln_fg_b,
+                         ln_q_g, ln_q_b, w_q, ln_qbg_g, ln_qbg_b, w_qbg,
+                         w_grid, ws, bank);
     } else {
       hipLaunchKernelGGL((k_main<1>), dim3(64,16), dim3(256), 0, stream,
-                         feat_color, ln_fc_g, ln_fc_b, w_pos, ws);
+                         feat_color, ln_fc_g, ln_fc_b, w_pos, ws, bank);
       hipLaunchKernelGGL(k_final, dim3(5,16), dim3(64), 0, stream,
                          w_mlp_fg, b_mlp_fg, w_mlp_bg, b_mlp_bg,
-                         ln_fg_g, ln_fg_b, ws, out);
-    }
-  }
-}
+                         ln_fg_g, ln_fg_b, w_grid, ws, out);
+    }
+  }
+}
```

Measured after the change: 246.4 us. 20.8% more time.
